# Optimization experiments

Hardware: AMD Instinct MI355X
Metric: run time of the kernel (lower is better)

## Reference

```python
import jax, jax.numpy as jnp
import numpy as np

B, C, H, W = 4, 64, 128, 128
O, K = 64, 3
STRIDE, PAD = 1, 1
K2 = K * K


def conv2d(x, w, b):
    out = jax.lax.conv_general_dilated(
        x, w, (STRIDE, STRIDE), [(PAD, PAD), (PAD, PAD)],
        dimension_numbers=('NCHW', 'OIHW', 'NCHW'))
    return out + b[None, :, None, None]


def setup_inputs() -> dict:
    key = jax.random.key(0)
    ks = jax.random.split(key, 6)
    return {
        'x': jax.random.normal(ks[0], (B, C, H, W), jnp.float32),
        'offset_w': jax.random.normal(ks[1], (2 * K2, C, K, K), jnp.float32) * 0.01,
        'offset_b': jax.random.normal(ks[2], (2 * K2,), jnp.float32) * 0.01,
        'mask_w': jax.random.normal(ks[3], (K2, C, K, K), jnp.float32) * 0.01,
        'mask_b': jnp.zeros((K2,), jnp.float32),
        'deform_w': jax.random.normal(ks[4], (O, C, K, K), jnp.float32) * (1.0 / np.sqrt(C * K2)),
        'deform_b': jax.random.normal(ks[5], (O,), jnp.float32) * 0.01,
    }


def _deform_conv(x, offset, mask, w, b):
    Bn, Cn, Hin, Win = x.shape
    Ho, Wo = offset.shape[2], offset.shape[3]
    off = offset.reshape(Bn, K2, 2, Ho, Wo)
    ky = jnp.repeat(jnp.arange(K), K)   # kernel row offset per location k
    kx = jnp.tile(jnp.arange(K), K)     # kernel col offset per location k
    yo = jnp.arange(Ho) * STRIDE - PAD
    xo = jnp.arange(Wo) * STRIDE - PAD
    # sampling positions [B,K2,Ho,Wo]
    py = off[:, :, 0] + ky[None, :, None, None] + yo[None, None, :, None]
    px = off[:, :, 1] + kx[None, :, None, None] + xo[None, None, None, :]
    y0 = jnp.floor(py)
    x0 = jnp.floor(px)
    wy1 = py - y0  # fractional weights
    wx1 = px - x0
    y0i = y0.astype(jnp.int32)
    x0i = x0.astype(jnp.int32)
    x_flat = x.reshape(Bn, Cn, Hin * Win)

    def corner(yi, xi, wgt):
        valid = (yi >= 0) & (yi < Hin) & (xi >= 0) & (xi < Win)
        yc = jnp.clip(yi, 0, Hin - 1)
        xc = jnp.clip(xi, 0, Win - 1)
        idx = (yc * Win + xc).reshape(Bn, -1)
        g = jnp.take_along_axis(x_flat, idx[:, None, :], axis=2)
        g = g.reshape(Bn, Cn, K2, Ho, Wo)
        return g * (wgt * valid)[:, None]

    val = (corner(y0i, x0i, (1 - wy1) * (1 - wx1))
           + corner(y0i, x0i + 1, (1 - wy1) * wx1)
           + corner(y0i + 1, x0i, wy1 * (1 - wx1))
           + corner(y0i + 1, x0i + 1, wy1 * wx1))
    val = val * mask[:, None]  # modulate, broadcast over channels
    out = jnp.einsum('bckhw,ock->bohw', val, w.reshape(w.shape[0], Cn, K2))
    return out + b[None, :, None, None]


def reference(x, offset_w, offset_b, mask_w, mask_b, deform_w, deform_b):
    offset = conv2d(x, offset_w, offset_b)
    mask = jax.nn.sigmoid(conv2d(x, mask_w, mask_b))
    return _deform_conv(x, offset, mask, deform_w, deform_b)
```

## Files before the change

kernel.cpp:

```cpp
#include <hip/hip_runtime.h>
#include <hip/hip_bf16.h>
#include <math.h>

#define BB 4
#define CC 64
#define HH 128
#define WW 128
#define HW 16384
#define CHW (CC*HW)

typedef __bf16 bf16;
typedef __attribute__((ext_vector_type(8))) __bf16 bf16x8;
typedef __attribute__((ext_vector_type(4))) __bf16 bf16x4;
typedef __attribute__((ext_vector_type(4))) float f32x4;
typedef __attribute__((ext_vector_type(4))) unsigned short u16x4;

#define MFMA(a, b, c) __builtin_amdgcn_mfma_f32_16x16x32_bf16((a), (b), (c), 0, 0, 0)

__global__ __launch_bounds__(256) void k_pre(const float* __restrict__ x,
        bf16* __restrict__ xt,
        const float* __restrict__ dw, const float* __restrict__ ow,
        const float* __restrict__ mw,
        bf16* __restrict__ wfd_hi, bf16* __restrict__ wfd_lo,
        bf16* __restrict__ wfo_hi, bf16* __restrict__ wfo_lo) {
    __shared__ float tile[64][65];
    if (blockIdx.x < 1024) {
        int b    = blockIdx.x >> 8;
        int s0   = (blockIdx.x & 255) * 64;
        int lane = threadIdx.x & 63;
        int w    = threadIdx.x >> 6;
        const float* xb = x + (size_t)b * CHW;
        #pragma unroll
        for (int r = 0; r < 16; ++r) {
            int c = w * 16 + r;
            tile[c][lane] = xb[(size_t)c * HW + s0 + lane];
        }
        __syncthreads();
        bf16* xtb = xt + (size_t)b * CHW;
        #pragma unroll
        for (int it = 0; it < 2; ++it) {
            int task = it * 256 + threadIdx.x;
            int s = task >> 3, ch0 = (task & 7) * 8;
            bf16x8 v;
            #pragma unroll
            for (int j = 0; j < 8; ++j) v[j] = (bf16)tile[ch0 + j][s];
            *(bf16x8*)&xtb[(size_t)(s0 + s) * 64 + ch0] = v;
        }
    } else {
        int idx = (blockIdx.x - 1024) * 256 + threadIdx.x;
        if (idx < 36864) {
            int j    = idx & 7;
            int lane = (idx >> 3) & 63;
            int ks   = (idx >> 9) % 18;
            int nt   = idx / (512 * 18);
            int n    = nt * 16 + (lane & 15);
            int kglob = ks * 32 + (lane >> 4) * 8 + j;
            int kk = kglob >> 6, c = kglob & 63;
            float w = dw[(n * 64 + c) * 9 + kk];
            bf16 h = (bf16)w;
            wfd_hi[idx] = h;
            wfd_lo[idx] = (bf16)(w - (float)h);
        } else {
            int idx2 = idx - 36864;
            int j    = idx2 & 7;
            int lane = (idx2 >> 3) & 63;
            int ks   = (idx2 >> 9) % 18;
            int nt   = idx2 / (512 * 18);
            int ch   = nt * 16 + (lane & 15);
            int kglob = ks * 32 + (lane >> 4) * 8 + j;
            int kk = kglob >> 6, c = kglob & 63;
            float w = 0.0f;
            if (ch < 18)      w = ow[(ch * 64 + c) * 9 + kk];
            else if (ch < 27) w = mw[((ch - 18) * 64 + c) * 9 + kk];
            bf16 h = (bf16)w;
            wfo_hi[idx2] = h;
            wfo_lo[idx2] = (bf16)(w - (float)h);
        }
    }
}

__global__ __launch_bounds__(256) void k_fused(const bf16* __restrict__ xt,
        const bf16* __restrict__ wfo_hi, const bf16* __restrict__ wfo_lo,
        const bf16* __restrict__ wfd_hi,
        const float* __restrict__ ob, const float* __restrict__ mb,
        const float* __restrict__ db, float* __restrict__ out) {
    __shared__ __align__(16) bf16 a_s2[2][18 * 64 * 8];
    __shared__ float om_s[27 * 64];
    __shared__ __align__(8) bf16 sampw[576 * 4];
    __shared__ __align__(8) unsigned short sampo[576 * 4];

    int bid = (blockIdx.x & 7) * 128 + (blockIdx.x >> 3);
    int pos0 = bid * 64;
    int wo0 = pos0 & 127;
    int ho  = (pos0 >> 7) & 127;
    int b   = pos0 >> 14;
    int t = threadIdx.x, wave = t >> 6, lane = t & 63;
    int m = lane & 15, g = lane >> 4;
    const bf16* xtb = xt + (size_t)b * CHW;

    {
        int st = wave;
        f32x4 acc0 = {0.f, 0.f, 0.f, 0.f};
        f32x4 acc1 = {0.f, 0.f, 0.f, 0.f};
        const bf16x8* bh0 = (const bf16x8*)wfo_hi + lane;
        const bf16x8* bl0 = (const bf16x8*)wfo_lo + lane;
        const bf16x8* bh1 = (const bf16x8*)wfo_hi + 18 * 64 + lane;
        const bf16x8* bl1 = (const bf16x8*)wfo_lo + 18 * 64 + lane;
        #pragma unroll
        for (int kk = 0; kk < 9; ++kk) {
            int y  = ho + kk / 3 - 1;
            int xx = wo0 + st * 16 + m + (kk % 3) - 1;
            bf16x8 ae = {};
            bf16x8 ao = {};
            if ((unsigned)y < 128u && (unsigned)xx < 128u) {
                const bf16* bp = xtb + ((size_t)(y * 128 + xx) << 6);
                ae = *(const bf16x8*)(bp + g * 8);
                ao = *(const bf16x8*)(bp + 32 + g * 8);
            }
            int ks0 = 2 * kk, ks1 = 2 * kk + 1;
            acc0 = MFMA(ae, bh0[ks0 * 64], acc0);
            acc0 = MFMA(ae, bl0[ks0 * 64], acc0);
            acc0 = MFMA(ao, bh0[ks1 * 64], acc0);
            acc0 = MFMA(ao, bl0[ks1 * 64], acc0);
            acc1 = MFMA(ae, bh1[ks0 * 64], acc1);
            acc1 = MFMA(ae, bl1[ks0 * 64], acc1);
            acc1 = MFMA(ao, bh1[ks1 * 64], acc1);
            acc1 = MFMA(ao, bl1[ks1 * 64], acc1);
        }
        int p64 = st * 16 + g * 4;
        float bias0 = ob[m];
        #pragma unroll
        for (int r = 0; r < 4; ++r)
            om_s[m * 64 + p64 + r] = acc0[r] + bias0;
        int ch1 = 16 + m;
        if (ch1 < 27) {
            float bias1 = (ch1 < 18) ? ob[ch1] : mb[ch1 - 18];
            #pragma unroll
            for (int r = 0; r < 4; ++r) {
                float v = acc1[r] + bias1;
                if (ch1 >= 18) v = 1.0f / (1.0f + __expf(-v));
                om_s[ch1 * 64 + p64 + r] = v;
            }
        }
    }
    __syncthreads();

    for (int task = t; task < 576; task += 256) {
        int p64 = task / 9, k = task - p64 * 9;
        float dy = om_s[(2 * k) * 64 + p64];
        float dx = om_s[(2 * k + 1) * 64 + p64];
        float mk = om_s[(18 + k) * 64 + p64];
        float py = (float)(ho - 1 + k / 3) + dy;
        float px = (float)(wo0 + p64 - 1 + (k % 3)) + dx;
        float y0f = floorf(py), x0f = floorf(px);
        float fy = py - y0f, fx = px - x0f;
        int y0 = (int)y0f, x0 = (int)x0f;
        int y1 = y0 + 1,  x1 = x0 + 1;
        bool vy0 = (unsigned)y0 < 128u, vy1 = (unsigned)y1 < 128u;
        bool vx0 = (unsigned)x0 < 128u, vx1 = (unsigned)x1 < 128u;
        int y0c = min(max(y0, 0), 127), y1c = min(max(y1, 0), 127);
        int x0c = min(max(x0, 0), 127), x1c = min(max(x1, 0), 127);
        bf16x4 wv;
        wv.x = (bf16)((vy0 && vx0) ? mk * (1.f - fy) * (1.f - fx) : 0.f);
        wv.y = (bf16)((vy0 && vx1) ? mk * (1.f - fy) * fx         : 0.f);
        wv.z = (bf16)((vy1 && vx0) ? mk * fy * (1.f - fx)         : 0.f);
        wv.w = (bf16)((vy1 && vx1) ? mk * fy * fx                 : 0.f);
        u16x4 ov;
        ov.x = (unsigned short)(y0c * 128 + x0c);
        ov.y = (unsigned short)(y0c * 128 + x1c);
        ov.z = (unsigned short)(y1c * 128 + x0c);
        ov.w = (unsigned short)(y1c * 128 + x1c);
        *(bf16x4*)&sampw[task * 4] = wv;
        *(u16x4*)&sampo[task * 4] = ov;
    }
    __syncthreads();

    const bf16x8* bhd = (const bf16x8*)wfd_hi + (size_t)wave * 18 * 64 + lane;
    int fle = ((m ^ g) + (g << 4)) * 8;
    int flo = ((m ^ g ^ 4) + (g << 4)) * 8;
    int half = t >> 7;
    int prow = (t >> 3) & 15;
    int c8   = (t & 7) * 8;
    int kpar = c8 >> 5;
    int gch  = (c8 & 31) >> 3;
    int flw  = (prow ^ gch ^ (kpar << 2)) + (gch << 4);
    char* abw = (char*)&a_s2[half][0] + (flw << 4);

    #pragma unroll
    for (int sp = 0; sp < 2; ++sp) {
        int stc = sp * 2 + half;
        int taskbase = (stc * 16 + prow) * 9;
        #pragma unroll
        for (int kk = 0; kk < 9; ++kk) {
            int task = taskbase + kk;
            bf16x4 wb = *(const bf16x4*)&sampw[task * 4];
            u16x4  o4 = *(const u16x4*)&sampo[task * 4];
            bf16x8 v00 = *(const bf16x8*)&xtb[((int)o4.x << 6) + c8];
            bf16x8 v01 = *(const bf16x8*)&xtb[((int)o4.y << 6) + c8];
            bf16x8 v10 = *(const bf16x8*)&xtb[((int)o4.z << 6) + c8];
            bf16x8 v11 = *(const bf16x8*)&xtb[((int)o4.w << 6) + c8];
            float w00 = (float)wb.x, w01 = (float)wb.y;
            float w10 = (float)wb.z, w11 = (float)wb.w;
            bf16x8 hv;
            #pragma unroll
            for (int j = 0; j < 8; ++j) {
                float r = w00 * (float)v00[j] + w01 * (float)v01[j]
                        + w10 * (float)v10[j] + w11 * (float)v11[j];
                hv[j] = (bf16)r;
            }
            int ks = 2 * kk + kpar;
            *(bf16x8*)(abw + (ks << 10)) = hv;
        }
        __syncthreads();

        #pragma unroll
        for (int h2 = 0; h2 < 2; ++h2) {
            int st = sp * 2 + h2;
            const bf16* ab = &a_s2[h2][0];
            f32x4 acc = {0.f, 0.f, 0.f, 0.f};
            __builtin_amdgcn_s_setprio(1);
            #pragma unroll
            for (int kk = 0; kk < 9; ++kk) {
                bf16x8 a0 = *(const bf16x8*)&ab[(2 * kk) * 512 + fle];
                bf16x8 a1 = *(const bf16x8*)&ab[(2 * kk + 1) * 512 + flo];
                acc = MFMA(a0, bhd[(2 * kk) * 64], acc);
                acc = MFMA(a1, bhd[(2 * kk + 1) * 64], acc);
            }
            __builtin_amdgcn_s_setprio(0);
            int o = wave * 16 + m;
            float bias = db[o];
            float4 vv = {acc[0] + bias, acc[1] + bias, acc[2] + bias, acc[3] + bias};
            *(float4*)&out[((size_t)(b * 64 + o)) * HW + ho * 128 + wo0 + st * 16 + g * 4] = vv;
        }
        if (sp == 0) __syncthreads();
    }
}

extern "C" void kernel_launch(void* const* d_in, const int* in_sizes, int n_in,
                              void* d_out, int out_size, void* d_ws, size_t ws_size,
                              hipStream_t stream) {
    const float* x   = (const float*)d_in[0];
    const float* ow  = (const float*)d_in[1];
    const float* ob  = (const float*)d_in[2];
    const float* mw  = (const float*)d_in[3];
    const float* mb  = (const float*)d_in[4];
    const float* dw  = (const float*)d_in[5];
    const float* db  = (const float*)d_in[6];
    float* out = (float*)d_out;

    bf16* xt = (bf16*)d_ws;
    bf16* wfd_hi = xt + (size_t)BB * HW * CC;
    bf16* wfd_lo = wfd_hi + 36864;
    bf16* wfo_hi = wfd_lo + 36864;
    bf16* wfo_lo = wfo_hi + 18432;

    k_pre<<<1024 + 216, 256, 0, stream>>>(x, xt, dw, ow, mw, wfd_hi, wfd_lo, wfo_hi, wfo_lo);
    k_fused<<<(BB * HW) / 64, 256, 0, stream>>>(xt, wfo_hi, wfo_lo, wfd_hi, ob, mb, db, out);
}
```

Before: 121.7 us.

## Split fused deform-conv kernel into offset/mask kernel and gather-GEMM kernel

Splits the fused kernel in two. The first kernel computes the offset/mask conv and writes bilinear sampling weights and indices to global workspace. The second reads them back, gathers and interpolates into one shared A tile per 16-position strip, and runs the MFMA GEMM. The gather work per strip is split across the two thread halves by kernel tap (5/4) instead of by strip. The aim is lower shared-memory and register pressure so more blocks fit per CU, at the cost of an extra launch, a global round trip for the sampling tables, and more barriers.

```diff
diff --git a/kernel.cpp b/kernel.cpp
--- a/kernel.cpp
+++ b/kernel.cpp
@@ -79,15 +79,11 @@
     }
 }
 
-__global__ __launch_bounds__(256) void k_fused(const bf16* __restrict__ xt,
+__global__ __launch_bounds__(256) void k_B(const bf16* __restrict__ xt,
         const bf16* __restrict__ wfo_hi, const bf16* __restrict__ wfo_lo,
-        const bf16* __restrict__ wfd_hi,
         const float* __restrict__ ob, const float* __restrict__ mb,
-        const float* __restrict__ db, float* __restrict__ out) {
-    __shared__ __align__(16) bf16 a_s2[2][18 * 64 * 8];
+        bf16* __restrict__ sampw_g, unsigned short* __restrict__ sampo_g) {
     __shared__ float om_s[27 * 64];
-    __shared__ __align__(8) bf16 sampw[576 * 4];
-    __shared__ __align__(8) unsigned short sampo[576 * 4];
 
     int bid = (blockIdx.x & 7) * 128 + (blockIdx.x >> 3);
     int pos0 = bid * 64;
@@ -145,6 +141,8 @@
     }
     __syncthreads();
 
+    bf16* swg = sampw_g + (size_t)bid * 576 * 4;
+    unsigned short* sog = sampo_g + (size_t)bid * 576 * 4;
     for (int task = t; task < 576; task += 256) {
         int p64 = task / 9, k = task - p64 * 9;
         float dy = om_s[(2 * k) * 64 + p64];
@@ -170,31 +168,46 @@
         ov.y = (unsigned short)(y0c * 128 + x1c);
         ov.z = (unsigned short)(y1c * 128 + x0c);
         ov.w = (unsigned short)(y1c * 128 + x1c);
-        *(bf16x4*)&sampw[task * 4] = wv;
-        *(u16x4*)&sampo[task * 4] = ov;
-    }
-    __syncthreads();
+        *(bf16x4*)&swg[task * 4] = wv;
+        *(u16x4*)&sog[task * 4] = ov;
+    }
+}
+
+__global__ __launch_bounds__(256) void k_D(const bf16* __restrict__ xt,
+        const bf16* __restrict__ wfd_hi,
+        const bf16* __restrict__ sampw_g, const unsigned short* __restrict__ sampo_g,
+        const float* __restrict__ db, float* __restrict__ out) {
+    __shared__ __align__(16) bf16 a_s[18 * 64 * 8];
+
+    int bid = (blockIdx.x & 7) * 128 + (blockIdx.x >> 3);
+    int pos0 = bid * 64;
+    int wo0 = pos0 & 127;
+    int ho  = (pos0 >> 7) & 127;
+    int b   = pos0 >> 14;
+    int t = threadIdx.x, wave = t >> 6, lane = t & 63;
+    int m = lane & 15, g = lane >> 4;
+    const bf16* xtb = xt + (size_t)b * CHW;
 
     const bf16x8* bhd = (const bf16x8*)wfd_hi + (size_t)wave * 18 * 64 + lane;
     int fle = ((m ^ g) + (g << 4)) * 8;
     int flo = ((m ^ g ^ 4) + (g << 4)) * 8;
-    int half = t >> 7;
-    int prow = (t >> 3) & 15;
-    int c8   = (t & 7) * 8;
-    int kpar = c8 >> 5;
-    int gch  = (c8 & 31) >> 3;
-    int flw  = (prow ^ gch ^ (kpar << 2)) + (gch << 4);
-    char* abw = (char*)&a_s2[half][0] + (flw << 4);
-
-    #pragma unroll
-    for (int sp = 0; sp < 2; ++sp) {
-        int stc = sp * 2 + half;
-        int taskbase = (stc * 16 + prow) * 9;
-        #pragma unroll
-        for (int kk = 0; kk < 9; ++kk) {
+
+    int khalf = t >> 7;
+    int prow  = (t >> 3) & 15;
+    int c8    = (t & 7) * 8;
+    int kpar  = c8 >> 5;
+    int gch   = (c8 & 31) >> 3;
+    int flw   = (prow ^ gch ^ (kpar << 2)) + (gch << 4);
+    char* abw = (char*)a_s + (flw << 4);
+    const bf16* swb = sampw_g + (size_t)bid * 576 * 4;
+    const unsigned short* sob = sampo_g + (size_t)bid * 576 * 4;
+
+    for (int st = 0; st < 4; ++st) {
+        int taskbase = (st * 16 + prow) * 9;
+        auto gather1 = [&](int kk) {
             int task = taskbase + kk;
-            bf16x4 wb = *(const bf16x4*)&sampw[task * 4];
-            u16x4  o4 = *(const u16x4*)&sampo[task * 4];
+            bf16x4 wb = *(const bf16x4*)&swb[task * 4];
+            u16x4  o4 = *(const u16x4*)&sob[task * 4];
             bf16x8 v00 = *(const bf16x8*)&xtb[((int)o4.x << 6) + c8];
             bf16x8 v01 = *(const bf16x8*)&xtb[((int)o4.y << 6) + c8];
             bf16x8 v10 = *(const bf16x8*)&xtb[((int)o4.z << 6) + c8];
@@ -210,29 +223,31 @@
             }
             int ks = 2 * kk + kpar;
             *(bf16x8*)(abw + (ks << 10)) = hv;
+        };
+        if (!khalf) {
+            #pragma unroll
+            for (int kk = 0; kk < 5; ++kk) gather1(kk);
+        } else {
+            #pragma unroll
+            for (int kk = 5; kk < 9; ++kk) gather1(kk);
         }
         __syncthreads();
 
-        #pragma unroll
-        for (int h2 = 0; h2 < 2; ++h2) {
-            int st = sp * 2 + h2;
-            const bf16* ab = &a_s2[h2][0];
-            f32x4 acc = {0.f, 0.f, 0.f, 0.f};
-            __builtin_amdgcn_s_setprio(1);
-            #pragma unroll
-            for (int kk = 0; kk < 9; ++kk) {
-                bf16x8 a0 = *(const bf16x8*)&ab[(2 * kk) * 512 + fle];
-                bf16x8 a1 = *(const bf16x8*)&ab[(2 * kk + 1) * 512 + flo];
-                acc = MFMA(a0, bhd[(2 * kk) * 64], acc);
-                acc = MFMA(a1, bhd[(2 * kk + 1) * 64], acc);
-            }
-            __builtin_amdgcn_s_setprio(0);
-            int o = wave * 16 + m;
-            float bias = db[o];
-            float4 vv = {acc[0] + bias, acc[1] + bias, acc[2] + bias, acc[3] + bias};
-            *(float4*)&out[((size_t)(b * 64 + o)) * HW + ho * 128 + wo0 + st * 16 + g * 4] = vv;
-        }
-        if (sp == 0) __syncthreads();
+        f32x4 acc = {0.f, 0.f, 0.f, 0.f};
+        __builtin_amdgcn_s_setprio(1);
+        #pragma unroll
+        for (int kk = 0; kk < 9; ++kk) {
+            bf16x8 a0 = *(const bf16x8*)&a_s[(2 * kk) * 512 + fle];
+            bf16x8 a1 = *(const bf16x8*)&a_s[(2 * kk + 1) * 512 + flo];
+            acc = MFMA(a0, bhd[(2 * kk) * 64], acc);
+            acc = MFMA(a1, bhd[(2 * kk + 1) * 64], acc);
+        }
+        __builtin_amdgcn_s_setprio(0);
+        int o = wave * 16 + m;
+        float bias = db[o];
+        float4 vv = {acc[0] + bias, acc[1] + bias, acc[2] + bias, acc[3] + bias};
+        *(float4*)&out[((size_t)(b * 64 + o)) * HW + ho * 128 + wo0 + st * 16 + g * 4] = vv;
+        if (st < 3) __syncthreads();
     }
 }
 
@@ -253,7 +268,10 @@
     bf16* wfd_lo = wfd_hi + 36864;
     bf16* wfo_hi = wfd_lo + 36864;
     bf16* wfo_lo = wfo_hi + 18432;
+    bf16* sampw_g = wfo_lo + 18432;
+    unsigned short* sampo_g = (unsigned short*)(sampw_g + (size_t)1024 * 576 * 4);
 
     k_pre<<<1024 + 216, 256, 0, stream>>>(x, xt, dw, ow, mw, wfd_hi, wfd_lo, wfo_hi, wfo_lo);
-    k_fused<<<(BB * HW) / 64, 256, 0, stream>>>(xt, wfo_hi, wfo_lo, wfd_hi, ob, mb, db, out);
-}
+    k_B<<<1024, 256, 0, stream>>>(xt, wfo_hi, wfo_lo, ob, mb, sampw_g, sampo_g);
+    k_D<<<1024, 256, 0, stream>>>(xt, wfd_hi, sampw_g, sampo_g, db, out);
+}
```

Measured after the change: 124.9 us. 1.03x slower.

## Software-pipeline bilinear gathers, interleave MFMA chains, vectorize transpose pre-pass

Applied to the files above, without the earlier changes.

The bilinear sampling loop now double-buffers sample metadata and corner gathers one tap ahead, so global-load latency overlaps the interpolation arithmetic. The MFMA stage runs two independent accumulator chains across both A tiles and shares the B fragment loads, which shortens dependent MFMA chains and removes the setprio calls. The x transpose pre-kernel now uses float4 loads on 32-column tiles with twice as many blocks. The cost is higher register pressure from the prefetch buffers, which could lower occupancy.

```diff
diff --git a/kernel.cpp b/kernel.cpp
--- a/kernel.cpp
+++ b/kernel.cpp
@@ -23,31 +23,34 @@
         const float* __restrict__ mw,
         bf16* __restrict__ wfd_hi, bf16* __restrict__ wfd_lo,
         bf16* __restrict__ wfo_hi, bf16* __restrict__ wfo_lo) {
-    __shared__ float tile[64][65];
-    if (blockIdx.x < 1024) {
-        int b    = blockIdx.x >> 8;
-        int s0   = (blockIdx.x & 255) * 64;
-        int lane = threadIdx.x & 63;
-        int w    = threadIdx.x >> 6;
+    __shared__ float tile[64][33];
+    if (blockIdx.x < 2048) {
+        int b    = blockIdx.x >> 9;
+        int s0   = (blockIdx.x & 511) * 32;
+        int t    = threadIdx.x;
         const float* xb = x + (size_t)b * CHW;
         #pragma unroll
-        for (int r = 0; r < 16; ++r) {
-            int c = w * 16 + r;
-            tile[c][lane] = xb[(size_t)c * HW + s0 + lane];
+        for (int it = 0; it < 2; ++it) {
+            int task = it * 256 + t;
+            int c    = task >> 3;
+            int col4 = (task & 7) * 4;
+            float4 v = *(const float4*)&xb[(size_t)c * HW + s0 + col4];
+            tile[c][col4 + 0] = v.x;
+            tile[c][col4 + 1] = v.y;
+            tile[c][col4 + 2] = v.z;
+            tile[c][col4 + 3] = v.w;
         }
         __syncthreads();
         bf16* xtb = xt + (size_t)b * CHW;
-        #pragma unroll
-        for (int it = 0; it < 2; ++it) {
-            int task = it * 256 + threadIdx.x;
-            int s = task >> 3, ch0 = (task & 7) * 8;
+        {
+            int s = t >> 3, ch0 = (t & 7) * 8;
             bf16x8 v;
             #pragma unroll
             for (int j = 0; j < 8; ++j) v[j] = (bf16)tile[ch0 + j][s];
             *(bf16x8*)&xtb[(size_t)(s0 + s) * 64 + ch0] = v;
         }
     } else {
-        int idx = (blockIdx.x - 1024) * 256 + threadIdx.x;
+        int idx = (blockIdx.x - 2048) * 256 + threadIdx.x;
         if (idx < 36864) {
             int j    = idx & 7;
             int lane = (idx >> 3) & 63;
@@ -188,49 +191,72 @@
 
     #pragma unroll
     for (int sp = 0; sp < 2; ++sp) {
-        int stc = sp * 2 + half;
-        int taskbase = (stc * 16 + prow) * 9;
-        #pragma unroll
-        for (int kk = 0; kk < 9; ++kk) {
-            int task = taskbase + kk;
-            bf16x4 wb = *(const bf16x4*)&sampw[task * 4];
-            u16x4  o4 = *(const u16x4*)&sampo[task * 4];
-            bf16x8 v00 = *(const bf16x8*)&xtb[((int)o4.x << 6) + c8];
-            bf16x8 v01 = *(const bf16x8*)&xtb[((int)o4.y << 6) + c8];
-            bf16x8 v10 = *(const bf16x8*)&xtb[((int)o4.z << 6) + c8];
-            bf16x8 v11 = *(const bf16x8*)&xtb[((int)o4.w << 6) + c8];
-            float w00 = (float)wb.x, w01 = (float)wb.y;
-            float w10 = (float)wb.z, w11 = (float)wb.w;
-            bf16x8 hv;
-            #pragma unroll
-            for (int j = 0; j < 8; ++j) {
-                float r = w00 * (float)v00[j] + w01 * (float)v01[j]
-                        + w10 * (float)v10[j] + w11 * (float)v11[j];
-                hv[j] = (bf16)r;
-            }
-            int ks = 2 * kk + kpar;
-            *(bf16x8*)(abw + (ks << 10)) = hv;
+        {
+            int stc = sp * 2 + half;
+            int taskbase = (stc * 16 + prow) * 9;
+            bf16x4 wbuf[2]; u16x4 obuf[2]; bf16x8 cbuf[2][4];
+            auto ldsamp = [&](int kk) {
+                int tk = taskbase + kk;
+                wbuf[kk & 1] = *(const bf16x4*)&sampw[tk * 4];
+                obuf[kk & 1] = *(const u16x4*)&sampo[tk * 4];
+            };
+            auto ldcor = [&](int kk) {
+                u16x4 o = obuf[kk & 1];
+                cbuf[kk & 1][0] = *(const bf16x8*)&xtb[((int)o.x << 6) + c8];
+                cbuf[kk & 1][1] = *(const bf16x8*)&xtb[((int)o.y << 6) + c8];
+                cbuf[kk & 1][2] = *(const bf16x8*)&xtb[((int)o.z << 6) + c8];
+                cbuf[kk & 1][3] = *(const bf16x8*)&xtb[((int)o.w << 6) + c8];
+            };
+            auto docompute = [&](int kk) {
+                bf16x4 wv = wbuf[kk & 1];
+                float w00 = (float)wv.x, w01 = (float)wv.y;
+                float w10 = (float)wv.z, w11 = (float)wv.w;
+                bf16x8 hv;
+                #pragma unroll
+                for (int j = 0; j < 8; ++j) {
+                    float r = w00 * (float)cbuf[kk & 1][0][j]
+                            + w01 * (float)cbuf[kk & 1][1][j]
+                            + w10 * (float)cbuf[kk & 1][2][j]
+                            + w11 * (float)cbuf[kk & 1][3][j];
+                    hv[j] = (bf16)r;
+                }
+                int ks = 2 * kk + kpar;
+                *(bf16x8*)(abw + (ks << 10)) = hv;
+            };
+            ldsamp(0); ldcor(0); ldsamp(1);
+            #pragma unroll
+            for (int kk = 0; kk < 9; ++kk) {
+                if (kk < 8) ldcor(kk + 1);
+                docompute(kk);
+                if (kk < 7) ldsamp(kk + 2);
+            }
         }
         __syncthreads();
 
-        #pragma unroll
-        for (int h2 = 0; h2 < 2; ++h2) {
-            int st = sp * 2 + h2;
-            const bf16* ab = &a_s2[h2][0];
-            f32x4 acc = {0.f, 0.f, 0.f, 0.f};
-            __builtin_amdgcn_s_setprio(1);
+        {
+            f32x4 acc0 = {0.f, 0.f, 0.f, 0.f};
+            f32x4 acc1 = {0.f, 0.f, 0.f, 0.f};
             #pragma unroll
             for (int kk = 0; kk < 9; ++kk) {
-                bf16x8 a0 = *(const bf16x8*)&ab[(2 * kk) * 512 + fle];
-                bf16x8 a1 = *(const bf16x8*)&ab[(2 * kk + 1) * 512 + flo];
-                acc = MFMA(a0, bhd[(2 * kk) * 64], acc);
-                acc = MFMA(a1, bhd[(2 * kk + 1) * 64], acc);
-            }
-            __builtin_amdgcn_s_setprio(0);
+                bf16x8 b0 = bhd[(2 * kk) * 64];
+                bf16x8 b1 = bhd[(2 * kk + 1) * 64];
+                bf16x8 a0e = *(const bf16x8*)&a_s2[0][(2 * kk) * 512 + fle];
+                bf16x8 a0o = *(const bf16x8*)&a_s2[0][(2 * kk + 1) * 512 + flo];
+                bf16x8 a1e = *(const bf16x8*)&a_s2[1][(2 * kk) * 512 + fle];
+                bf16x8 a1o = *(const bf16x8*)&a_s2[1][(2 * kk + 1) * 512 + flo];
+                acc0 = MFMA(a0e, b0, acc0);
+                acc1 = MFMA(a1e, b0, acc1);
+                acc0 = MFMA(a0o, b1, acc0);
+                acc1 = MFMA(a1o, b1, acc1);
+            }
             int o = wave * 16 + m;
             float bias = db[o];
-            float4 vv = {acc[0] + bias, acc[1] + bias, acc[2] + bias, acc[3] + bias};
-            *(float4*)&out[((size_t)(b * 64 + o)) * HW + ho * 128 + wo0 + st * 16 + g * 4] = vv;
+            int st0 = sp * 2;
+            float4 v0 = {acc0[0] + bias, acc0[1] + bias, acc0[2] + bias, acc0[3] + bias};
+            float4 v1 = {acc1[0] + bias, acc1[1] + bias, acc1[2] + bias, acc1[3] + bias};
+            size_t obase = ((size_t)(b * 64 + o)) * HW + ho * 128 + wo0 + g * 4;
+            *(float4*)&out[obase + st0 * 16] = v0;
+            *(float4*)&out[obase + (st0 + 1) * 16] = v1;
         }
         if (sp == 0) __syncthreads();
     }
@@ -254,6 +280,6 @@
     bf16* wfo_hi = wfd_lo + 36864;
     bf16* wfo_lo = wfo_hi + 18432;
 
-    k_pre<<<1024 + 216, 256, 0, stream>>>(x, xt, dw, ow, mw, wfd_hi, wfd_lo, wfo_hi, wfo_lo);
+    k_pre<<<2048 + 216, 256, 0, stream>>>(x, xt, dw, ow, mw, wfd_hi, wfd_lo, wfo_hi, wfo_lo);
     k_fused<<<(BB * HW) / 64, 256, 0, stream>>>(xt, wfo_hi, wfo_lo, wfd_hi, ob, mb, db, out);
 }
```

New measurement: 120.1 us. No clear change (-1.3%).
